# Kernel optimization log

Measured on AMD Instinct MI355X. Metric: run time of the kernel, lower is better.

The kernel has to match this reference:

```python
import jax, jax.numpy as jnp
import numpy as np

WS = (7, 7)      # window_size
SS = (3, 3)      # shift_size
NH = 6           # num_heads


def _rel_index(ws):
    # Faithful to define_relative_position_index (including its quirk of
    # summing raw signed offsets, which can be negative -> wraparound gather).
    coords = jnp.stack(jnp.meshgrid(jnp.arange(ws[0]), jnp.arange(ws[1]), indexing='ij'))  # (2,w0,w1)
    flat = coords.reshape(2, -1)                       # (2,N)
    rel = flat[:, :, None] - flat[:, None, :]          # (2,N,N)
    return rel.sum(axis=0).reshape(-1)                 # (N*N,)


def setup_inputs() -> dict:
    key = jax.random.key(0)
    ks = jax.random.split(key, 6)
    C, H, W = 192, 448, 448
    return {
        'x': jax.random.normal(ks[0], (C, H, W), dtype=jnp.float32),
        'qkv_weight': jax.random.normal(ks[1], (3 * C, C), dtype=jnp.float32) * 0.05,
        'qkv_bias': jax.random.normal(ks[2], (3 * C,), dtype=jnp.float32) * 0.02,
        'proj_weight': jax.random.normal(ks[3], (C, C), dtype=jnp.float32) * 0.05,
        'proj_bias': jax.random.normal(ks[4], (C,), dtype=jnp.float32) * 0.02,
        'rel_bias_table': jax.random.normal(ks[5], ((2 * WS[0] - 1) * (2 * WS[1] - 1), NH), dtype=jnp.float32) * 0.02,
    }


def reference(x, qkv_weight, qkv_bias, proj_weight, proj_bias, rel_bias_table):
    C, H, W = x.shape
    w0, w1 = WS
    s0, s1 = SS
    N = w0 * w1
    hd = C // NH
    nW = (H // w0) * (W // w1)

    # relative position bias: (NH, N, N)
    idx = _rel_index(WS)
    bias = rel_bias_table[idx].reshape(N, N, NH).transpose(2, 0, 1)

    xh = jnp.transpose(x, (1, 2, 0))                          # (H,W,C)
    xh = jnp.roll(xh, (-s0, -s1), axis=(0, 1))                # cyclic shift
    xw = xh.reshape(H // w0, w0, W // w1, w1, C)
    xw = xw.transpose(0, 2, 1, 3, 4).reshape(nW, N, C)        # window partition

    qkv = xw @ qkv_weight.T + qkv_bias                        # (nW,N,3C)
    qkv = qkv.reshape(nW, N, 3, NH, hd).transpose(2, 0, 3, 1, 4)
    q = qkv[0] * (hd ** -0.5)
    k = qkv[1]
    v = qkv[2]

    attn = jnp.einsum('whnd,whmd->whnm', q, k) + bias         # (nW,NH,N,N)

    # shift attention mask (region buckets 0..8, value row*3+col)
    rb = (jnp.arange(H) >= H - w0).astype(jnp.int32) + (jnp.arange(H) >= H - s0).astype(jnp.int32)
    cb = (jnp.arange(W) >= W - w1).astype(jnp.int32) + (jnp.arange(W) >= W - s1).astype(jnp.int32)
    img = rb[:, None] * 3 + cb[None, :]                       # (H,W)
    m = img.reshape(H // w0, w0, W // w1, w1).transpose(0, 2, 1, 3).reshape(nW, N)
    amask = jnp.where(m[:, None, :] - m[:, :, None] == 0, 0.0, -100.0)  # (nW,N,N)
    attn = attn + amask[:, None, :, :]

    attn = jax.nn.softmax(attn, axis=-1)                      # attention_dropout p=0 -> identity

    out = jnp.einsum('whnm,whmd->whnd', attn, v)              # (nW,NH,N,hd)
    out = out.transpose(0, 2, 1, 3).reshape(nW, N, C)
    out = out @ proj_weight.T + proj_bias                     # dropout p=0 -> identity

    out = out.reshape(H // w0, W // w1, w0, w1, C)
    out = out.transpose(0, 2, 1, 3, 4).reshape(H, W, C)       # reverse window partition
    out = jnp.roll(out, (s0, s1), axis=(0, 1))                # reverse cyclic shift
    return jnp.transpose(out, (2, 0, 1))                      # back to (C,H,W)
```

## Files before the change

### kernel.cpp

```cpp
#include <hip/hip_runtime.h>


typedef short s16x8 __attribute__((ext_vector_type(8)));
typedef float f32x4 __attribute__((ext_vector_type(4)));
typedef unsigned short u16x4 __attribute__((ext_vector_type(4)));

#define C_DIM 192
#define H_DIM 448
#define W_DIM 448
#define HW    (H_DIM * W_DIM)
#define NHEAD 6
#define NTOK  49
#define MT    64

#define XW_S 200
#define AO_S 200
#define QH_S 40
#define KH_S 40
#define VT_S 72
#define PH_S 72

__device__ __forceinline__ unsigned short f2bf(float f) {
  unsigned u = __float_as_uint(f);
  u = (u + 0x7fffu + ((u >> 16) & 1u)) >> 16;
  return (unsigned short)u;
}

__device__ __forceinline__ void gl_lds16(const void* g, void* l) {
  __builtin_amdgcn_global_load_lds(
      (const __attribute__((address_space(1))) void*)g,
      (__attribute__((address_space(3))) void*)l, 16, 0, 0);
}

__global__ void pack_wqkv(const float* __restrict__ w, unsigned short* __restrict__ dst) {
  int g = blockIdx.x * blockDim.x + threadIdx.x;
  if (g >= 13824) return;
  int lane = g & 63;
  int t1 = g >> 6;
  int kk = t1 % 6;  t1 /= 6;
  int dt = t1 & 1;  t1 >>= 1;
  int which = t1 % 3;
  int h = t1 / 3;
  int n  = which * 192 + h * 32 + dt * 16 + (lane & 15);
  int kb = kk * 32 + (lane >> 4) * 8;
  const float* src = w + n * 192 + kb;
  unsigned short* d = dst + g * 8;
#pragma unroll
  for (int j = 0; j < 8; j++) d[j] = f2bf(src[j]);
}

__global__ void pack_wproj(const float* __restrict__ w, unsigned short* __restrict__ dst) {
  int g = blockIdx.x * blockDim.x + threadIdx.x;
  if (g >= 4608) return;
  int lane = g & 63;
  int t1 = g >> 6;
  int kk = t1 % 6;
  int nt = t1 / 6;
  int n  = nt * 16 + (lane & 15);
  int kb = kk * 32 + (lane >> 4) * 8;
  const float* src = w + n * 192 + kb;
  unsigned short* d = dst + g * 8;
#pragma unroll
  for (int j = 0; j < 8; j++) d[j] = f2bf(src[j]);
}

__global__ void bias_prep(const float* __restrict__ table, float* __restrict__ dst) {
  int t = blockIdx.x * blockDim.x + threadIdx.x;
  if (t >= 6 * 64 * 64) return;
  int j = t & 63;
  int i = (t >> 6) & 63;
  int h = t >> 12;
  float v = 0.f;
  if (i < NTOK && j < NTOK) {
    int s = (i / 7 - j / 7) + (i % 7 - j % 7);
    if (s < 0) s += 169;
    v = table[s * 6 + h];
  }
  dst[t] = v;
}

__global__ __launch_bounds__(256) void transpose_in(
    const float* __restrict__ x, unsigned short* __restrict__ xT) {
  __shared__ __align__(16) unsigned short tile[64 * XW_S];
  const int hw0 = blockIdx.x * 64;
  const int col = threadIdx.x & 63;
  const int hw = hw0 + col;
#pragma unroll 8
  for (int c = threadIdx.x >> 6; c < 192; c += 4)
    tile[col * XW_S + c] = f2bf(x[c * HW + hw]);
  __syncthreads();
  const int r = hw0 / W_DIM;
  const int wbase = hw0 % W_DIM;
  int rp = r + (H_DIM - 3); if (rp >= H_DIM) rp -= H_DIM;
  for (int t = threadIdx.x; t < 64 * 24; t += 256) {
    int cc = t / 24, c8 = t % 24;
    int w = wbase + cc;
    int wp = w + (W_DIM - 3); if (wp >= W_DIM) wp -= W_DIM;
    *(s16x8*)(xT + ((rp * W_DIM + wp) * 192 + c8 * 8)) =
        *(const s16x8*)&tile[cc * XW_S + c8 * 8];
  }
}

template <int MODE>
__global__ __launch_bounds__(256) void transpose_out(
    const void* __restrict__ oT, float* __restrict__ out) {
  __shared__ __align__(16) float tile[64 * 196];
  const int hw0 = blockIdx.x * 64;
  if (MODE == 0) {
    const float* p = (const float*)oT;
    for (int t = threadIdx.x; t < 64 * 48; t += 256) {
      int cc = t / 48, c4 = t % 48;
      *(f32x4*)&tile[cc * 196 + c4 * 4] =
          *(const f32x4*)(p + (hw0 + cc) * 192 + c4 * 4);
    }
  } else {
    const unsigned short* p = (const unsigned short*)oT;
    for (int t = threadIdx.x; t < 64 * 24; t += 256) {
      int cc = t / 24, c8 = t % 24;
      s16x8 v = *(const s16x8*)(p + (hw0 + cc) * 192 + c8 * 8);
#pragma unroll
      for (int k = 0; k < 8; k++)
        tile[cc * 196 + c8 * 8 + k] =
            __uint_as_float(((unsigned)(unsigned short)v[k]) << 16);
    }
  }
  __syncthreads();
  const int col = threadIdx.x & 63;
#pragma unroll 8
  for (int c = threadIdx.x >> 6; c < 192; c += 4)
    out[c * HW + hw0 + col] = tile[col * 196 + c];
}

template <int MODE>
__global__ __launch_bounds__(256, 2) void swin_fused(
    const float* __restrict__ x,
    const unsigned short* __restrict__ xT,
    const float* __restrict__ qkv_bias,
    const float* __restrict__ proj_bias,
    const unsigned short* __restrict__ wqkv_p,
    const unsigned short* __restrict__ wproj_p,
    const float* __restrict__ biasM,
    void* __restrict__ outT,
    float* __restrict__ out) {
  __shared__ __align__(16) unsigned short xw[MT * XW_S];
  __shared__ __align__(16) unsigned short ao[MT * AO_S];
  __shared__ __align__(16) unsigned short qh[MT * QH_S];
  __shared__ __align__(16) unsigned short kh[MT * KH_S];
  __shared__ __align__(16) unsigned short vth[32 * VT_S];
  __shared__ __align__(16) unsigned short Ph[MT * PH_S];
  __shared__ int mreg[MT];

  const int tid  = threadIdx.x;
  const int lane = tid & 63;
  const int wid  = tid >> 6;
  const int l16  = lane & 15;
  const int quad = lane >> 4;
  const int wr   = blockIdx.x >> 6;
  const int wc   = blockIdx.x & 63;

  if (MODE != 3) {
    const unsigned short* xTw = xT + ((wr * 7) * W_DIM + wc * 7) * 192;
    for (int base = wid * 64; base < 1225; base += 256) {
      int t = base + lane;
      if (t < 1225) {
        int tok = t / 25, c8 = t % 25;
        int i = tok / 7, j = tok % 7;
        const unsigned short* g =
            (c8 == 24) ? xTw : xTw + (i * W_DIM + j) * 192 + c8 * 8;
        gl_lds16(g, &xw[base * 8]);
      }
    }
    s16x8 zz = {0, 0, 0, 0, 0, 0, 0, 0};
    for (int idx = tid; idx < 375; idx += 256)
      *(s16x8*)&xw[(1225 + idx) * 8] = zz;
  } else {
    for (int task = tid; task < 1344; task += 256) {
      int c = task / 7;
      int i = task % 7;
      int r = wr * 7 + i + 3; if (r >= H_DIM) r -= H_DIM;
      const float* src = x + c * HW + r * W_DIM;
      int cb = wc * 7 + 3;
#pragma unroll
      for (int j = 0; j < 7; j++) {
        int w = cb + j; if (w >= W_DIM) w -= W_DIM;
        xw[(i * 7 + j) * XW_S + c] = f2bf(src[w]);
      }
    }
    for (int idx = tid; idx < 15 * C_DIM; idx += 256)
      xw[(NTOK + idx / C_DIM) * XW_S + (idx % C_DIM)] = 0;
  }
  if (tid < MT) {
    int v = 99;
    if (tid < NTOK) {
      int gi = wr * 7 + tid / 7, gj = wc * 7 + tid % 7;
      int rb = (gi >= 441) + (gi >= 445);
      int cb = (gj >= 441) + (gj >= 445);
      v = rb * 3 + cb;
    }
    mreg[tid] = v;
  }
  __syncthreads();

  const float scale = 0.17677669529663687f;

  for (int h = 0; h < NHEAD; h++) {
    for (int e = wid; e < 6; e += 4) {
      int which = e >> 1;
      int dt = e & 1;
      s16x8 bf[6];
      const s16x8* wp = (const s16x8*)wqkv_p;
      int base = (((h * 3 + which) * 2 + dt) * 6) * 64 + lane;
#pragma unroll
      for (int kk = 0; kk < 6; kk++) bf[kk] = wp[base + kk * 64];
      int ncol = which * 192 + h * 32 + dt * 16 + l16;
      float bias = qkv_bias[ncol];
      int dl = dt * 16 + l16;
#pragma unroll
      for (int mt = 0; mt < 4; mt++) {
        f32x4 acc = {0.f, 0.f, 0.f, 0.f};
#pragma unroll
        for (int kk = 0; kk < 6; kk++) {
          s16x8 a = *(const s16x8*)&xw[(mt * 16 + l16) * XW_S + kk * 32 + quad * 8];
          acc = __builtin_amdgcn_mfma_f32_16x16x32_bf16(a, bf[kk], acc, 0, 0, 0);
        }
        int t0 = mt * 16 + quad * 4;
        if (which == 0) {
#pragma unroll
          for (int r = 0; r < 4; r++) qh[(t0 + r) * QH_S + dl] = f2bf(acc[r] + bias);
        } else if (which == 1) {
#pragma unroll
          for (int r = 0; r < 4; r++) kh[(t0 + r) * KH_S + dl] = f2bf(acc[r] + bias);
        } else {
          u16x4 pv;
#pragma unroll
          for (int r = 0; r < 4; r++) pv[r] = f2bf(acc[r] + bias);
          *(u16x4*)&vth[dl * VT_S + t0] = pv;
        }
      }
    }
    __syncthreads();

    {
      const int mt = wid;
      s16x8 aq = *(const s16x8*)&qh[(mt * 16 + l16) * QH_S + quad * 8];
      f32x4 sc[4];
#pragma unroll
      for (int nt = 0; nt < 4; nt++) {
        s16x8 bk = *(const s16x8*)&kh[(nt * 16 + l16) * KH_S + quad * 8];
        f32x4 z = {0.f, 0.f, 0.f, 0.f};
        sc[nt] = __builtin_amdgcn_mfma_f32_16x16x32_bf16(aq, bk, z, 0, 0, 0);
      }
      float sv[4][4];
#pragma unroll
      for (int nt = 0; nt < 4; nt++) {
        int j = nt * 16 + l16;
        int mj = mreg[j];
        float mpad = (j >= NTOK) ? -30000.f : 0.f;
#pragma unroll
        for (int r = 0; r < 4; r++) {
          int i = mt * 16 + quad * 4 + r;
          float s = sc[nt][r] * scale + biasM[(h * 64 + i) * 64 + j];
          s += (mreg[i] == mj) ? 0.f : -100.f;
          sv[r][nt] = s + mpad;
        }
      }
#pragma unroll
      for (int r = 0; r < 4; r++) {
        float mx = fmaxf(fmaxf(sv[r][0], sv[r][1]), fmaxf(sv[r][2], sv[r][3]));
#pragma unroll
        for (int off = 1; off < 16; off <<= 1) mx = fmaxf(mx, __shfl_xor(mx, off));
        float e0 = __expf(sv[r][0] - mx), e1 = __expf(sv[r][1] - mx);
        float e2 = __expf(sv[r][2] - mx), e3 = __expf(sv[r][3] - mx);
        float sm = e0 + e1 + e2 + e3;
#pragma unroll
        for (int off = 1; off < 16; off <<= 1) sm += __shfl_xor(sm, off);
        float inv = 1.f / sm;
        int i = mt * 16 + quad * 4 + r;
        Ph[i * PH_S +  0 + l16] = f2bf(e0 * inv);
        Ph[i * PH_S + 16 + l16] = f2bf(e1 * inv);
        Ph[i * PH_S + 32 + l16] = f2bf(e2 * inv);
        Ph[i * PH_S + 48 + l16] = f2bf(e3 * inv);
      }
    }

    {
      const int mt = wid;
      s16x8 ap0 = *(const s16x8*)&Ph[(mt * 16 + l16) * PH_S + quad * 8];
      s16x8 ap1 = *(const s16x8*)&Ph[(mt * 16 + l16) * PH_S + 32 + quad * 8];
#pragma unroll
      for (int dtv = 0; dtv < 2; dtv++) {
        s16x8 bv0 = *(const s16x8*)&vth[(dtv * 16 + l16) * VT_S + quad * 8];
        s16x8 bv1 = *(const s16x8*)&vth[(dtv * 16 + l16) * VT_S + 32 + quad * 8];
        f32x4 acc = {0.f, 0.f, 0.f, 0.f};
        acc = __builtin_amdgcn_mfma_f32_16x16x32_bf16(ap0, bv0, acc, 0, 0, 0);
        acc = __builtin_amdgcn_mfma_f32_16x16x32_bf16(ap1, bv1, acc, 0, 0, 0);
        int t0 = mt * 16 + quad * 4;
#pragma unroll
        for (int r = 0; r < 4; r++)
          ao[(t0 + r) * AO_S + h * 32 + dtv * 16 + l16] = f2bf(acc[r]);
      }
    }
    __syncthreads();
  }

  for (int nt = wid; nt < 12; nt += 4) {
    s16x8 bf[6];
    const s16x8* wp = (const s16x8*)wproj_p;
    int base = nt * 6 * 64 + lane;
#pragma unroll
    for (int kk = 0; kk < 6; kk++) bf[kk] = wp[base + kk * 64];
    int cout = nt * 16 + l16;
    float pb = proj_bias[cout];
#pragma unroll
    for (int mt = 0; mt < 4; mt++) {
      f32x4 acc = {0.f, 0.f, 0.f, 0.f};
#pragma unroll
      for (int kk = 0; kk < 6; kk++) {
        s16x8 a = *(const s16x8*)&ao[(mt * 16 + l16) * AO_S + kk * 32 + quad * 8];
        acc = __builtin_amdgcn_mfma_f32_16x16x32_bf16(a, bf[kk], acc, 0, 0, 0);
      }
      int t0 = mt * 16 + quad * 4;
#pragma unroll
      for (int r = 0; r < 4; r++) {
        int t = t0 + r;
        if (t < NTOK) {
          int i = t / 7, j = t % 7;
          int R = wr * 7 + i + 3;  if (R >= H_DIM) R -= H_DIM;
          int Cc = wc * 7 + j + 3; if (Cc >= W_DIM) Cc -= W_DIM;
          float v = acc[r] + pb;
          if (MODE == 2 || MODE == 3) {
            out[cout * HW + R * W_DIM + Cc] = v;
          } else if (MODE == 0) {
            ((float*)outT)[(R * W_DIM + Cc) * 192 + cout] = v;
          } else {
            ((unsigned short*)outT)[(R * W_DIM + Cc) * 192 + cout] = f2bf(v);
          }
        }
      }
    }
  }
}

extern "C" void kernel_launch(void* const* d_in, const int* in_sizes, int n_in,
                              void* d_out, int out_size, void* d_ws, size_t ws_size,
                              hipStream_t stream) {
  const float* x     = (const float*)d_in[0];
  const float* wqkv  = (const float*)d_in[1];
  const float* bqkv  = (const float*)d_in[2];
  const float* wproj = (const float*)d_in[3];
  const float* bproj = (const float*)d_in[4];
  const float* table = (const float*)d_in[5];
  float* out = (float*)d_out;

  unsigned short* wqkv_p = (unsigned short*)d_ws;
  unsigned short* wproj_p = wqkv_p + 110592;
  float* biasM = (float*)(wproj_p + 36864);
  const size_t base_b = 393216;
  const size_t xT_b = (size_t)HW * 192 * 2;
  const size_t oT32_b = (size_t)HW * 192 * 4;
  unsigned short* xT = (unsigned short*)((char*)d_ws + base_b);
  void* outT = (char*)d_ws + base_b + xT_b;

  int mode;
  if (ws_size >= base_b + xT_b + oT32_b) mode = 0;
  else if (ws_size >= base_b + xT_b + xT_b) mode = 1;
  else if (ws_size >= base_b + xT_b) mode = 2;
  else mode = 3;

  pack_wqkv<<<54, 256, 0, stream>>>(wqkv, wqkv_p);
  pack_wproj<<<18, 256, 0, stream>>>(wproj, wproj_p);
  bias_prep<<<96, 256, 0, stream>>>(table, biasM);
  if (mode != 3)
    transpose_in<<<HW / 64, 256, 0, stream>>>(x, xT);

  switch (mode) {
    case 0:
      swin_fused<0><<<4096, 256, 0, stream>>>(x, xT, bqkv, bproj, wqkv_p,
                                              wproj_p, biasM, outT, out);
      transpose_out<0><<<HW / 64, 256, 0, stream>>>(outT, out);
      break;
    case 1:
      swin_fused<1><<<4096, 256, 0, stream>>>(x, xT, bqkv, bproj, wqkv_p,
                                              wproj_p, biasM, outT, out);
      transpose_out<1><<<HW / 64, 256, 0, stream>>>(outT, out);
      break;
    case 2:
      swin_fused<2><<<4096, 256, 0, stream>>>(x, xT, bqkv, bproj, wqkv_p,
                                              wproj_p, biasM, outT, out);
      break;
    default:
      swin_fused<3><<<4096, 256, 0, stream>>>(x, xT, bqkv, bproj, wqkv_p,
                                              wproj_p, biasM, outT, out);
      break;
  }
}
```

Measured before the change: 583.6 us.

## Fold Q scale into weights, drop softmax max, rebalance QKV work, swizzle blocks

Pre-multiplies the query weights and bias by the attention scale and folds the padding mask into the bias table. Softmax now skips the max reduction, and the shift mask is applied only for edge windows. QKV projection work is spread evenly across the four warps (six tile units each) so each A fragment is reused for two outputs. The input transpose uses vectorized float4 loads with a rotated LDS layout over 128-pixel tiles, block indices are swizzled for locality, and the bf16 intermediate mode is removed. Dropping the max subtraction relies on small logits to avoid overflow in exp.

```diff
diff --git a/kernel.cpp b/kernel.cpp
--- a/kernel.cpp
+++ b/kernel.cpp
@@ -12,6 +12,7 @@
 #define NHEAD 6
 #define NTOK  49
 #define MT    64
+#define QSCALE 0.17677669529663687f
 
 #define XW_S 200
 #define AO_S 200
@@ -45,8 +46,9 @@
   int kb = kk * 32 + (lane >> 4) * 8;
   const float* src = w + n * 192 + kb;
   unsigned short* d = dst + g * 8;
-#pragma unroll
-  for (int j = 0; j < 8; j++) d[j] = f2bf(src[j]);
+  float m = (which == 0) ? QSCALE : 1.f;
+#pragma unroll
+  for (int j = 0; j < 8; j++) d[j] = f2bf(src[j] * m);
 }
 
 __global__ void pack_wproj(const float* __restrict__ w, unsigned short* __restrict__ dst) {
@@ -70,8 +72,10 @@
   int j = t & 63;
   int i = (t >> 6) & 63;
   int h = t >> 12;
-  float v = 0.f;
-  if (i < NTOK && j < NTOK) {
+  float v;
+  if (j >= NTOK) v = -30000.f;
+  else if (i >= NTOK) v = 0.f;
+  else {
     int s = (i / 7 - j / 7) + (i % 7 - j % 7);
     if (s < 0) s += 169;
     v = table[s * 6 + h];
@@ -81,54 +85,47 @@
 
 __global__ __launch_bounds__(256) void transpose_in(
     const float* __restrict__ x, unsigned short* __restrict__ xT) {
-  __shared__ __align__(16) unsigned short tile[64 * XW_S];
-  const int hw0 = blockIdx.x * 64;
-  const int col = threadIdx.x & 63;
-  const int hw = hw0 + col;
-#pragma unroll 8
-  for (int c = threadIdx.x >> 6; c < 192; c += 4)
-    tile[col * XW_S + c] = f2bf(x[c * HW + hw]);
+  __shared__ __align__(16) unsigned short tile[128 * 200];
+  const int hw0 = blockIdx.x * 128;
+  for (int u = threadIdx.x; u < 192 * 32; u += 256) {
+    int c = u >> 5, l32 = u & 31;
+    int hl = l32 * 4;
+    f32x4 v = *(const f32x4*)(x + (size_t)c * HW + hw0 + hl);
+    int c8 = c >> 3, o = c & 7;
+#pragma unroll
+    for (int i = 0; i < 4; i++) {
+      int hh = hl + i;
+      int rot = c8 + hh; rot %= 25;
+      tile[hh * 200 + rot * 8 + o] = f2bf(v[i]);
+    }
+  }
   __syncthreads();
-  const int r = hw0 / W_DIM;
-  const int wbase = hw0 % W_DIM;
-  int rp = r + (H_DIM - 3); if (rp >= H_DIM) rp -= H_DIM;
-  for (int t = threadIdx.x; t < 64 * 24; t += 256) {
-    int cc = t / 24, c8 = t % 24;
-    int w = wbase + cc;
+  for (int u = threadIdx.x; u < 128 * 24; u += 256) {
+    int t = u / 24, k = u % 24;
+    int hw = hw0 + t;
+    int r = hw / W_DIM, w = hw - r * W_DIM;
+    int rp = r + (H_DIM - 3); if (rp >= H_DIM) rp -= H_DIM;
     int wp = w + (W_DIM - 3); if (wp >= W_DIM) wp -= W_DIM;
-    *(s16x8*)(xT + ((rp * W_DIM + wp) * 192 + c8 * 8)) =
-        *(const s16x8*)&tile[cc * XW_S + c8 * 8];
-  }
-}
-
-template <int MODE>
+    int rot = k + t; rot %= 25;
+    *(s16x8*)(xT + ((size_t)(rp * W_DIM + wp) * 192 + k * 8)) =
+        *(const s16x8*)&tile[t * 200 + rot * 8];
+  }
+}
+
 __global__ __launch_bounds__(256) void transpose_out(
-    const void* __restrict__ oT, float* __restrict__ out) {
+    const float* __restrict__ oT, float* __restrict__ out) {
   __shared__ __align__(16) float tile[64 * 196];
   const int hw0 = blockIdx.x * 64;
-  if (MODE == 0) {
-    const float* p = (const float*)oT;
-    for (int t = threadIdx.x; t < 64 * 48; t += 256) {
-      int cc = t / 48, c4 = t % 48;
-      *(f32x4*)&tile[cc * 196 + c4 * 4] =
-          *(const f32x4*)(p + (hw0 + cc) * 192 + c4 * 4);
-    }
-  } else {
-    const unsigned short* p = (const unsigned short*)oT;
-    for (int t = threadIdx.x; t < 64 * 24; t += 256) {
-      int cc = t / 24, c8 = t % 24;
-      s16x8 v = *(const s16x8*)(p + (hw0 + cc) * 192 + c8 * 8);
-#pragma unroll
-      for (int k = 0; k < 8; k++)
-        tile[cc * 196 + c8 * 8 + k] =
-            __uint_as_float(((unsigned)(unsigned short)v[k]) << 16);
-    }
+  for (int t = threadIdx.x; t < 64 * 48; t += 256) {
+    int cc = t / 48, c4 = t % 48;
+    *(f32x4*)&tile[cc * 196 + c4 * 4] =
+        *(const f32x4*)(oT + (size_t)(hw0 + cc) * 192 + c4 * 4);
   }
   __syncthreads();
   const int col = threadIdx.x & 63;
 #pragma unroll 8
   for (int c = threadIdx.x >> 6; c < 192; c += 4)
-    out[c * HW + hw0 + col] = tile[col * 196 + c];
+    out[(size_t)c * HW + hw0 + col] = tile[col * 196 + c];
 }
 
 template <int MODE>
@@ -140,7 +137,7 @@
     const unsigned short* __restrict__ wqkv_p,
     const unsigned short* __restrict__ wproj_p,
     const float* __restrict__ biasM,
-    void* __restrict__ outT,
+    float* __restrict__ outT,
     float* __restrict__ out) {
   __shared__ __align__(16) unsigned short xw[MT * XW_S];
   __shared__ __align__(16) unsigned short ao[MT * AO_S];
@@ -155,18 +152,20 @@
   const int wid  = tid >> 6;
   const int l16  = lane & 15;
   const int quad = lane >> 4;
-  const int wr   = blockIdx.x >> 6;
-  const int wc   = blockIdx.x & 63;
+  const int wix  = ((blockIdx.x & 7) << 9) | (blockIdx.x >> 3);
+  const int wr   = wix >> 6;
+  const int wc   = wix & 63;
+  const bool edge = (wr == 63) || (wc == 63);
 
   if (MODE != 3) {
-    const unsigned short* xTw = xT + ((wr * 7) * W_DIM + wc * 7) * 192;
+    const unsigned short* xTw = xT + ((size_t)(wr * 7) * W_DIM + wc * 7) * 192;
     for (int base = wid * 64; base < 1225; base += 256) {
       int t = base + lane;
       if (t < 1225) {
         int tok = t / 25, c8 = t % 25;
         int i = tok / 7, j = tok % 7;
         const unsigned short* g =
-            (c8 == 24) ? xTw : xTw + (i * W_DIM + j) * 192 + c8 * 8;
+            (c8 == 24) ? xTw : xTw + ((size_t)(i * W_DIM + j)) * 192 + c8 * 8;
         gl_lds16(g, &xw[base * 8]);
       }
     }
@@ -178,7 +177,7 @@
       int c = task / 7;
       int i = task % 7;
       int r = wr * 7 + i + 3; if (r >= H_DIM) r -= H_DIM;
-      const float* src = x + c * HW + r * W_DIM;
+      const float* src = x + (size_t)c * HW + r * W_DIM;
       int cb = wc * 7 + 3;
 #pragma unroll
       for (int j = 0; j < 7; j++) {
@@ -201,40 +200,75 @@
   }
   __syncthreads();
 
-  const float scale = 0.17677669529663687f;
+  const int ubase = wid * 6;
+  const int eA = ubase >> 2, mtA0 = ubase & 3;
+  const int cntA = 4 - mtA0;
+  const int eB = eA + 1, cntB = 6 - cntA;
 
   for (int h = 0; h < NHEAD; h++) {
-    for (int e = wid; e < 6; e += 4) {
-      int which = e >> 1;
-      int dt = e & 1;
-      s16x8 bf[6];
+    {
       const s16x8* wp = (const s16x8*)wqkv_p;
-      int base = (((h * 3 + which) * 2 + dt) * 6) * 64 + lane;
-#pragma unroll
-      for (int kk = 0; kk < 6; kk++) bf[kk] = wp[base + kk * 64];
-      int ncol = which * 192 + h * 32 + dt * 16 + l16;
-      float bias = qkv_bias[ncol];
-      int dl = dt * 16 + l16;
+      s16x8 bfA[6], bfB[6];
+      const int whA = eA >> 1, dtA = eA & 1;
+      const int whB = eB >> 1, dtB = eB & 1;
+      const int baseA = (((h * 3 + whA) * 2 + dtA) * 6) * 64 + lane;
+      const int baseB = (((h * 3 + whB) * 2 + dtB) * 6) * 64 + lane;
+#pragma unroll
+      for (int kk = 0; kk < 6; kk++) {
+        bfA[kk] = wp[baseA + kk * 64];
+        bfB[kk] = wp[baseB + kk * 64];
+      }
+      float biasA = qkv_bias[whA * 192 + h * 32 + dtA * 16 + l16];
+      float biasB = qkv_bias[whB * 192 + h * 32 + dtB * 16 + l16];
+      if (whA == 0) biasA *= QSCALE;
+      if (whB == 0) biasB *= QSCALE;
+
 #pragma unroll
       for (int mt = 0; mt < 4; mt++) {
-        f32x4 acc = {0.f, 0.f, 0.f, 0.f};
-#pragma unroll
-        for (int kk = 0; kk < 6; kk++) {
-          s16x8 a = *(const s16x8*)&xw[(mt * 16 + l16) * XW_S + kk * 32 + quad * 8];
-          acc = __builtin_amdgcn_mfma_f32_16x16x32_bf16(a, bf[kk], acc, 0, 0, 0);
+        const bool inA = (mt >= mtA0);
+        const bool inB = (mt < cntB);
+        s16x8 a[6];
+#pragma unroll
+        for (int kk = 0; kk < 6; kk++)
+          a[kk] = *(const s16x8*)&xw[(mt * 16 + l16) * XW_S + kk * 32 + quad * 8];
+        const int t0 = mt * 16 + quad * 4;
+        if (inA) {
+          f32x4 acc = {0.f, 0.f, 0.f, 0.f};
+#pragma unroll
+          for (int kk = 0; kk < 6; kk++)
+            acc = __builtin_amdgcn_mfma_f32_16x16x32_bf16(a[kk], bfA[kk], acc, 0, 0, 0);
+          const int dl = dtA * 16 + l16;
+          if (whA == 0) {
+#pragma unroll
+            for (int r = 0; r < 4; r++) qh[(t0 + r) * QH_S + dl] = f2bf(acc[r] + biasA);
+          } else if (whA == 1) {
+#pragma unroll
+            for (int r = 0; r < 4; r++) kh[(t0 + r) * KH_S + dl] = f2bf(acc[r] + biasA);
+          } else {
+            u16x4 pv;
+#pragma unroll
+            for (int r = 0; r < 4; r++) pv[r] = f2bf(acc[r] + biasA);
+            *(u16x4*)&vth[dl * VT_S + t0] = pv;
+          }
         }
-        int t0 = mt * 16 + quad * 4;
-        if (which == 0) {
-#pragma unroll
-          for (int r = 0; r < 4; r++) qh[(t0 + r) * QH_S + dl] = f2bf(acc[r] + bias);
-        } else if (which == 1) {
-#pragma unroll
-          for (int r = 0; r < 4; r++) kh[(t0 + r) * KH_S + dl] = f2bf(acc[r] + bias);
-        } else {
-          u16x4 pv;
-#pragma unroll
-          for (int r = 0; r < 4; r++) pv[r] = f2bf(acc[r] + bias);
-          *(u16x4*)&vth[dl * VT_S + t0] = pv;
+        if (inB) {
+          f32x4 acc = {0.f, 0.f, 0.f, 0.f};
+#pragma unroll
+          for (int kk = 0; kk < 6; kk++)
+            acc = __builtin_amdgcn_mfma_f32_16x16x32_bf16(a[kk], bfB[kk], acc, 0, 0, 0);
+          const int dl = dtB * 16 + l16;
+          if (whB == 0) {
+#pragma unroll
+            for (int r = 0; r < 4; r++) qh[(t0 + r) * QH_S + dl] = f2bf(acc[r] + biasB);
+          } else if (whB == 1) {
+#pragma unroll
+            for (int r = 0; r < 4; r++) kh[(t0 + r) * KH_S + dl] = f2bf(acc[r] + biasB);
+          } else {
+            u16x4 pv;
+#pragma unroll
+            for (int r = 0; r < 4; r++) pv[r] = f2bf(acc[r] + biasB);
+            *(u16x4*)&vth[dl * VT_S + t0] = pv;
+          }
         }
       }
     }
@@ -242,6 +276,13 @@
 
     {
       const int mt = wid;
+      const float* bMh = biasM + ((h * 64 + mt * 16 + quad * 4) * 64) + l16;
+      float bm[4][4];
+#pragma unroll
+      for (int nt = 0; nt < 4; nt++)
+#pragma unroll
+        for (int r = 0; r < 4; r++) bm[nt][r] = bMh[r * 64 + nt * 16];
+
       s16x8 aq = *(const s16x8*)&qh[(mt * 16 + l16) * QH_S + quad * 8];
       f32x4 sc[4];
 #pragma unroll
@@ -250,28 +291,24 @@
         f32x4 z = {0.f, 0.f, 0.f, 0.f};
         sc[nt] = __builtin_amdgcn_mfma_f32_16x16x32_bf16(aq, bk, z, 0, 0, 0);
       }
-      float sv[4][4];
-#pragma unroll
-      for (int nt = 0; nt < 4; nt++) {
-        int j = nt * 16 + l16;
-        int mj = mreg[j];
-        float mpad = (j >= NTOK) ? -30000.f : 0.f;
-#pragma unroll
-        for (int r = 0; r < 4; r++) {
-          int i = mt * 16 + quad * 4 + r;
-          float s = sc[nt][r] * scale + biasM[(h * 64 + i) * 64 + j];
-          s += (mreg[i] == mj) ? 0.f : -100.f;
-          sv[r][nt] = s + mpad;
+      if (edge) {
+#pragma unroll
+        for (int nt = 0; nt < 4; nt++) {
+          int mj = mreg[nt * 16 + l16];
+#pragma unroll
+          for (int r = 0; r < 4; r++) {
+            int i = mt * 16 + quad * 4 + r;
+            bm[nt][r] += (mreg[i] == mj) ? 0.f : -100.f;
+          }
         }
       }
 #pragma unroll
       for (int r = 0; r < 4; r++) {
-        float mx = fmaxf(fmaxf(sv[r][0], sv[r][1]), fmaxf(sv[r][2], sv[r][3]));
-#pragma unroll
-        for (int off = 1; off < 16; off <<= 1) mx = fmaxf(mx, __shfl_xor(mx, off));
-        float e0 = __expf(sv[r][0] - mx), e1 = __expf(sv[r][1] - mx);
-        float e2 = __expf(sv[r][2] - mx), e3 = __expf(sv[r][3] - mx);
-        float sm = e0 + e1 + e2 + e3;
+        float e0 = __expf(sc[0][r] + bm[0][r]);
+        float e1 = __expf(sc[1][r] + bm[1][r]);
+        float e2 = __expf(sc[2][r] + bm[2][r]);
+        float e3 = __expf(sc[3][r] + bm[3][r]);
+        float sm = (e0 + e1) + (e2 + e3);
 #pragma unroll
         for (int off = 1; off < 16; off <<= 1) sm += __shfl_xor(sm, off);
         float inv = 1.f / sm;
@@ -328,12 +365,10 @@
           int R = wr * 7 + i + 3;  if (R >= H_DIM) R -= H_DIM;
           int Cc = wc * 7 + j + 3; if (Cc >= W_DIM) Cc -= W_DIM;
           float v = acc[r] + pb;
-          if (MODE == 2 || MODE == 3) {
-            out[cout * HW + R * W_DIM + Cc] = v;
-          } else if (MODE == 0) {
-            ((float*)outT)[(R * W_DIM + Cc) * 192 + cout] = v;
+          if (MODE == 0) {
+            outT[(size_t)(R * W_DIM + Cc) * 192 + cout] = v;
           } else {
-            ((unsigned short*)outT)[(R * W_DIM + Cc) * 192 + cout] = f2bf(v);
+            out[(size_t)cout * HW + R * W_DIM + Cc] = v;
           }
         }
       }
@@ -357,13 +392,12 @@
   float* biasM = (float*)(wproj_p + 36864);
   const size_t base_b = 393216;
   const size_t xT_b = (size_t)HW * 192 * 2;
-  const size_t oT32_b = (size_t)HW * 192 * 4;
+  const size_t oT_b = (size_t)HW * 192 * 4;
   unsigned short* xT = (unsigned short*)((char*)d_ws + base_b);
-  void* outT = (char*)d_ws + base_b + xT_b;
+  float* outT = (float*)((char*)d_ws + base_b + xT_b);
 
   int mode;
-  if (ws_size >= base_b + xT_b + oT32_b) mode = 0;
-  else if (ws_size >= base_b + xT_b + xT_b) mode = 1;
+  if (ws_size >= base_b + xT_b + oT_b) mode = 0;
   else if (ws_size >= base_b + xT_b) mode = 2;
   else mode = 3;
 
@@ -371,18 +405,13 @@
   pack_wproj<<<18, 256, 0, stream>>>(wproj, wproj_p);
   bias_prep<<<96, 256, 0, stream>>>(table, biasM);
   if (mode != 3)
-    transpose_in<<<HW / 64, 256, 0, stream>>>(x, xT);
+    transpose_in<<<HW / 128, 256, 0, stream>>>(x, xT);
 
   switch (mode) {
     case 0:
       swin_fused<0><<<4096, 256, 0, stream>>>(x, xT, bqkv, bproj, wqkv_p,
                                               wproj_p, biasM, outT, out);
-      transpose_out<0><<<HW / 64, 256, 0, stream>>>(outT, out);
-      break;
-    case 1:
-      swin_fused<1><<<4096, 256, 0, stream>>>(x, xT, bqkv, bproj, wqkv_p,
-                                              wproj_p, biasM, outT, out);
-      transpose_out<1><<<HW / 64, 256, 0, stream>>>(outT, out);
+      transpose_out<<<HW / 64, 256, 0, stream>>>(outT, out);
       break;
     case 2:
       swin_fused<2><<<4096, 256, 0, stream>>>(x, xT, bqkv, bproj, wqkv_p,
```

Result: faster. 542.1 us (-7.1%).
